# Performance work log

Measured on AMD Instinct MI355X. Metric: run time of the kernel, lower is better.

## Reference

```python
import jax, jax.numpy as jnp
import numpy as np

# dims: batch, internal ticks, neurons, input dim, NLM memory length, NLM hidden, sync pairs, out dims
B, T_TICKS, D, D_IN, M, H, P, D_OUT, D_ACT = 512, 8, 2048, 512, 16, 4, 512, 512, 512


def setup_inputs() -> dict:
    key = jax.random.key(0)
    ks = jax.random.split(key, 16)
    n = lambda k, shape: jax.random.normal(k, shape, dtype=jnp.float32)
    return {
        "x": n(ks[0], (B, D_IN)),
        # input projection
        "W_in": n(ks[1], (D_IN, D)) * 0.02,
        "b_in": jnp.zeros((D,), jnp.float32),
        # learned start post-activation state
        "z0": n(ks[2], (D,)) * 0.02,
        # synapse model: concat(z, features) -> pre-activations
        "W_syn": n(ks[3], (D + D, D)) * 0.02,
        "b_syn": jnp.zeros((D,), jnp.float32),
        # privately parameterized neuron-level models (NeuronLevelModel)
        "nlm_w1": n(ks[4], (M, H, D)) * 0.02,
        "nlm_b1": jnp.zeros((1, H, D), jnp.float32),
        "nlm_w2": n(ks[5], (H, D)) * 0.02,
        "nlm_b2": jnp.zeros((1, D), jnp.float32),
        # neural synchronization (NeuralSynchronization)
        "decay_out": jnp.zeros((P,), jnp.float32),
        "decay_action": jnp.zeros((P,), jnp.float32),
        "W_out": n(ks[6], (P, D_OUT)) * 0.02,
        "b_out": jnp.zeros((D_OUT,), jnp.float32),
        "W_act": n(ks[7], (P, D_ACT)) * 0.02,
        "b_act": jnp.zeros((D_ACT,), jnp.float32),
        # random neuron index pairs (buffers, int)
        "pairs_out": jax.random.randint(ks[8], (P, 2), 0, D),
        "pairs_action": jax.random.randint(ks[9], (P, 2), 0, D),
    }


def _nlm(hist, w1, b1, w2, b2):
    # hist: (B, D, M); private per-neuron 2-layer MLP
    h = jnp.einsum('bdM,Mhd->bdh', hist, w1) + jnp.swapaxes(b1, 1, 2)  # (B, D, H)
    h = jax.nn.relu(h)
    return jnp.einsum('bdh,hd->bd', h, w2) + b2  # (B, D)


def reference(x, W_in, b_in, z0, W_syn, b_syn, nlm_w1, nlm_b1, nlm_w2, nlm_b2,
              decay_out, decay_action, W_out, b_out, W_act, b_act,
              pairs_out, pairs_action):
    feats = x @ W_in + b_in                      # (B, D)
    z = jnp.broadcast_to(z0, (x.shape[0], D))    # (B, D)
    hist = jnp.zeros((x.shape[0], D, M), x.dtype)
    # exponential-decay sync recurrence: S_t = exp(-|r|) * S_{t-1} + z_i z_j
    # equals sum_s z_{i,s} z_{j,s} exp(-|r| (t - s))  (matches compute_sync weights)
    r_out = jnp.exp(-jnp.abs(decay_out))         # (P,)
    r_act = jnp.exp(-jnp.abs(decay_action))
    S_out = jnp.zeros((x.shape[0], P), x.dtype)
    S_act = jnp.zeros((x.shape[0], P), x.dtype)
    ys, qs = [], []
    for _ in range(T_TICKS):
        pre = jnp.concatenate([z, feats], axis=-1) @ W_syn + b_syn     # (B, D)
        hist = jnp.concatenate([hist[..., 1:], pre[..., None]], axis=-1)
        z = _nlm(hist, nlm_w1, nlm_b1, nlm_w2, nlm_b2)                 # (B, D)
        S_out = S_out * r_out + z[:, pairs_out[:, 0]] * z[:, pairs_out[:, 1]]
        S_act = S_act * r_act + z[:, pairs_action[:, 0]] * z[:, pairs_action[:, 1]]
        ys.append(S_out @ W_out + b_out)
        qs.append(S_act @ W_act + b_act)
    return jnp.stack(ys, axis=1), jnp.stack(qs, axis=1)  # (B, T, d_out), (B, T, d_action)
```

## Files before the change

kernel.cpp:

```cpp
#include <hip/hip_runtime.h>
#include <math.h>

#define Bsz 512
#define TT 8
#define Dn 2048
#define DIN 512
#define Hh 4
#define Pn 512
#define DOUT 512
#define BD (Bsz*Dn)

typedef __attribute__((ext_vector_type(8))) short s16x8;
typedef __attribute__((ext_vector_type(4))) float f32x4;
typedef __attribute__((ext_vector_type(4))) unsigned short u16x4;

__device__ __forceinline__ unsigned short f2bf(float f) {
  unsigned int u = __float_as_uint(f);
  unsigned int r = (u + 0x7fffu + ((u >> 16) & 1u)) >> 16;
  return (unsigned short)r;
}
__device__ __forceinline__ float bf2f(unsigned short h) {
  return __uint_as_float(((unsigned int)h) << 16);
}
__device__ __forceinline__ void split2(float x, unsigned short& h, unsigned short& l) {
  h = f2bf(x);
  float r = x - bf2f(h);
  l = f2bf(r);
}

#define GLOAD16(g, l) __builtin_amdgcn_global_load_lds( \
    (const __attribute__((address_space(1))) unsigned int*)(g), \
    (__attribute__((address_space(3))) unsigned int*)(l), 16, 0, 0)

__device__ __forceinline__ void gemm_core(
    const unsigned short* __restrict__ Ah, const unsigned short* __restrict__ Al,
    const unsigned short* __restrict__ BTh, const unsigned short* __restrict__ BTl,
    int K, long arow0, long brow0,
    unsigned short* LDS, f32x4 acc[2][2], int g, int qw)
{
  const int tid = threadIdx.x;
  const int lane = tid & 63;
  const int lh = lane >> 4, sc = lane & 15;
  const unsigned short* gsrc[8];
  int ldst[8];
#pragma unroll
  for (int t = 0; t < 4; ++t) {
    int rb = qw * 16 + t * 4;
    int row = rb + lh;
    int ko = ((sc & 7) ^ (row & 7)) << 3;
    gsrc[t]     = (sc >= 8 ? Al : Ah) + (size_t)(arow0 + row) * K + ko;
    ldst[t]     = rb * 128;
    gsrc[4 + t] = (sc >= 8 ? BTl : BTh) + (size_t)(brow0 + row) * K + ko;
    ldst[4 + t] = 32768 + rb * 128;
  }

  const int nI = K >> 7;

#define STAGE(ring, i_)                                              \
  {                                                                  \
    const size_t kb = ((size_t)(2 * (i_) + g)) << 6;                 \
    unsigned short* base = LDS + (g * 2 + (ring)) * 8192;            \
    GLOAD16(gsrc[0] + kb, base + ldst[0]);                           \
    GLOAD16(gsrc[1] + kb, base + ldst[1]);                           \
    GLOAD16(gsrc[2] + kb, base + ldst[2]);                           \
    GLOAD16(gsrc[3] + kb, base + ldst[3]);                           \
    GLOAD16(gsrc[4] + kb, base + ldst[4]);                           \
    GLOAD16(gsrc[5] + kb, base + ldst[5]);                           \
    GLOAD16(gsrc[6] + kb, base + ldst[6]);                           \
    GLOAD16(gsrc[7] + kb, base + ldst[7]);                           \
  }

  const int wm = (qw & 1) * 32, wn = (qw >> 1) * 32;
  const int lm = lane & 15, kg4 = lane >> 4;
  int aoh[2][2], boh[2][2];
#pragma unroll
  for (int u = 0; u < 2; ++u) {
    int kg = u * 4 + kg4;
#pragma unroll
    for (int mt = 0; mt < 2; ++mt) {
      int ar = wm + mt * 16 + lm;
      aoh[u][mt] = ar * 128 + ((kg ^ (ar & 7)) << 3);
    }
#pragma unroll
    for (int nt = 0; nt < 2; ++nt) {
      int br = wn + nt * 16 + lm;
      boh[u][nt] = br * 128 + ((kg ^ (br & 7)) << 3);
    }
  }

  STAGE(0, 0);
  for (int i = 0; i < nI; ++i) {
    asm volatile("s_waitcnt vmcnt(0)" ::: "memory");
    __builtin_amdgcn_s_barrier();
    if (i + 1 < nI) STAGE((i + 1) & 1, i + 1);
    const unsigned short* ab = LDS + (g * 2 + (i & 1)) * 8192;
    const unsigned short* bb = ab + 32768;
#pragma unroll
    for (int u = 0; u < 2; ++u) {
      s16x8 fah[2], fal[2], fbh[2], fbl[2];
#pragma unroll
      for (int mt = 0; mt < 2; ++mt) {
        fah[mt] = *(const s16x8*)(ab + aoh[u][mt]);
        fal[mt] = *(const s16x8*)(ab + aoh[u][mt] + 64);
      }
#pragma unroll
      for (int nt = 0; nt < 2; ++nt) {
        fbh[nt] = *(const s16x8*)(bb + boh[u][nt]);
        fbl[nt] = *(const s16x8*)(bb + boh[u][nt] + 64);
      }
      __builtin_amdgcn_s_setprio(1);
#pragma unroll
      for (int mt = 0; mt < 2; ++mt)
#pragma unroll
        for (int nt = 0; nt < 2; ++nt) {
          acc[mt][nt] = __builtin_amdgcn_mfma_f32_16x16x32_bf16(fah[mt], fbh[nt], acc[mt][nt], 0, 0, 0);
          acc[mt][nt] = __builtin_amdgcn_mfma_f32_16x16x32_bf16(fah[mt], fbl[nt], acc[mt][nt], 0, 0, 0);
          acc[mt][nt] = __builtin_amdgcn_mfma_f32_16x16x32_bf16(fal[mt], fbh[nt], acc[mt][nt], 0, 0, 0);
        }
      __builtin_amdgcn_s_setprio(0);
    }
  }
#undef STAGE

  __builtin_amdgcn_s_barrier();
  float* fred = (float*)LDS;
  const int ridx = (qw * 64 + lane) * 17;
  if (g == 1) {
#pragma unroll
    for (int mt = 0; mt < 2; ++mt)
#pragma unroll
      for (int nt = 0; nt < 2; ++nt)
#pragma unroll
        for (int r = 0; r < 4; ++r)
          fred[ridx + (mt * 2 + nt) * 4 + r] = acc[mt][nt][r];
  }
  __builtin_amdgcn_s_barrier();
  if (g == 0) {
#pragma unroll
    for (int mt = 0; mt < 2; ++mt)
#pragma unroll
      for (int nt = 0; nt < 2; ++nt)
#pragma unroll
        for (int r = 0; r < 4; ++r)
          acc[mt][nt][r] += fred[ridx + (mt * 2 + nt) * 4 + r];
  }
}

template<int MODE>
__global__ __launch_bounds__(512, 1)
void mfma_gemm(const unsigned short* __restrict__ Ah, const unsigned short* __restrict__ Al,
               const unsigned short* __restrict__ BTh, const unsigned short* __restrict__ BTl,
               const float* __restrict__ bias, float* __restrict__ Cf,
               unsigned short* __restrict__ Ch, unsigned short* __restrict__ Cl,
               int M, int N, int K, int gm, int gn)
{
  __shared__ unsigned short LDS[65536];
  int bid = blockIdx.x;
  int xcd = bid & 7, w = bid >> 3;
  int bmi = w % gm, bni = xcd * (gn >> 3) + w / gm;
  long bm = (long)bmi * 64, bn = (long)bni * 64;
  const int tid = threadIdx.x, lane = tid & 63, wave = tid >> 6;
  const int g = wave >> 2, qw = wave & 3;
  f32x4 acc[2][2];
#pragma unroll
  for (int a = 0; a < 2; ++a)
#pragma unroll
    for (int b = 0; b < 2; ++b) acc[a][b] = (f32x4)0.f;
  gemm_core(Ah, Al, BTh, BTl, K, bm, bn, LDS, acc, g, qw);
  if (g == 1) return;

  const int wm = (qw & 1) * 32, wn = (qw >> 1) * 32;
#pragma unroll
  for (int nt = 0; nt < 2; ++nt) {
    int n = (int)bn + wn + nt * 16 + (lane & 15);
    float bv = bias[n];
#pragma unroll
    for (int mt = 0; mt < 2; ++mt) {
      long r0 = bm + wm + mt * 16 + (lane >> 4) * 4;
#pragma unroll
      for (int r = 0; r < 4; ++r) {
        float v = acc[mt][nt][r] + bv;
        long R = r0 + r;
        if (MODE == 0) {
          unsigned short h_, l_; split2(v, h_, l_);
          Ch[R * N + n] = h_; Cl[R * N + n] = l_;
        } else if (MODE == 1) {
          Cf[R * N + n] = v;
        } else {
          long t = R >> 9, b = R & 511;
          Cf[(b * TT + t) * N + n] = v;
        }
      }
    }
  }
}

template<int TAU>
__global__ __launch_bounds__(512, 1)
void tick_mfma(const unsigned short* __restrict__ zh, const unsigned short* __restrict__ zl,
               const unsigned short* __restrict__ WTh, const unsigned short* __restrict__ WTl,
               const float* __restrict__ basep, const float* __restrict__ hist,
               float* __restrict__ histout,
               const float* __restrict__ w1, const float* __restrict__ b1,
               const float* __restrict__ w2, const float* __restrict__ b2,
               unsigned short* __restrict__ zho, unsigned short* __restrict__ zlo,
               unsigned short* __restrict__ zT)
{
  __shared__ unsigned short LDS[65536];
  int bid = blockIdx.x;
  int xcd = bid & 7, w = bid >> 3;
  int bmi = w % 8, bni = xcd * 4 + w / 8;
  long bm = (long)bmi * 64, bn = (long)bni * 64;
  const int tid = threadIdx.x, lane = tid & 63, wave = tid >> 6;
  const int g = wave >> 2, qw = wave & 3;
  f32x4 acc[2][2];
#pragma unroll
  for (int a = 0; a < 2; ++a)
#pragma unroll
    for (int b = 0; b < 2; ++b) acc[a][b] = (f32x4)0.f;
  gemm_core(zh, zl, WTh, WTl, Dn, bm, bn, LDS, acc, g, qw);
  if (g == 1) return;

  const int wm = (qw & 1) * 32, wn = (qw >> 1) * 32;
#pragma unroll
  for (int nt = 0; nt < 2; ++nt) {
    const int d = (int)bn + wn + nt * 16 + (lane & 15);
    float w2v[Hh], b1v[Hh];
#pragma unroll
    for (int hh = 0; hh < Hh; ++hh) {
      w2v[hh] = w2[hh * Dn + d];
      b1v[hh] = b1[hh * Dn + d];
    }
    const float b2v = b2[d];
#pragma unroll
    for (int mt = 0; mt < 2; ++mt) {
      const int b0 = (int)bm + wm + mt * 16 + (lane >> 4) * 4;
      float pre[4], hacc[4][Hh];
#pragma unroll
      for (int r = 0; r < 4; ++r) {
        pre[r] = acc[mt][nt][r] + basep[(size_t)(b0 + r) * Dn + d];
#pragma unroll
        for (int hh = 0; hh < Hh; ++hh) hacc[r][hh] = b1v[hh];
      }
#pragma unroll
      for (int s = 0; s < TAU; ++s) {
        float wv[Hh];
#pragma unroll
        for (int hh = 0; hh < Hh; ++hh) wv[hh] = w1[((15 - TAU + s) * Hh + hh) * Dn + d];
#pragma unroll
        for (int r = 0; r < 4; ++r) {
          float psv = hist[(size_t)s * BD + (size_t)(b0 + r) * Dn + d];
#pragma unroll
          for (int hh = 0; hh < Hh; ++hh) hacc[r][hh] = fmaf(psv, wv[hh], hacc[r][hh]);
        }
      }
      {
        float wv[Hh];
#pragma unroll
        for (int hh = 0; hh < Hh; ++hh) wv[hh] = w1[(15 * Hh + hh) * Dn + d];
#pragma unroll
        for (int r = 0; r < 4; ++r)
#pragma unroll
          for (int hh = 0; hh < Hh; ++hh) hacc[r][hh] = fmaf(pre[r], wv[hh], hacc[r][hh]);
      }
      u16x4 pack;
#pragma unroll
      for (int r = 0; r < 4; ++r) {
        histout[(size_t)(b0 + r) * Dn + d] = pre[r];
        float z = b2v;
#pragma unroll
        for (int hh = 0; hh < Hh; ++hh) z = fmaf(fmaxf(hacc[r][hh], 0.f), w2v[hh], z);
        unsigned short h_, l_; split2(z, h_, l_);
        zho[(size_t)(b0 + r) * Dn + d] = h_;
        zlo[(size_t)(b0 + r) * Dn + d] = l_;
        pack[r] = f2bf(z);
      }
      *(u16x4*)&zT[(size_t)d * Bsz + b0] = pack;
    }
  }
}

__global__ __launch_bounds__(256)
void tick0_kernel(const float* __restrict__ basep, const float* __restrict__ q,
                  float* __restrict__ histout,
                  const float* __restrict__ w1, const float* __restrict__ b1,
                  const float* __restrict__ w2, const float* __restrict__ b2,
                  unsigned short* __restrict__ zho, unsigned short* __restrict__ zlo,
                  unsigned short* __restrict__ zT)
{
  int g = blockIdx.x * 256 + threadIdx.x;
  int b = g >> 8;
  int d0 = (g & 255) * 8;
#pragma unroll
  for (int k = 0; k < 8; ++k) {
    int d = d0 + k;
    float pre = basep[(size_t)b * Dn + d] + q[d];
    histout[(size_t)b * Dn + d] = pre;
    float z = b2[d];
#pragma unroll
    for (int hh = 0; hh < Hh; ++hh) {
      float h = fmaf(pre, w1[(15 * Hh + hh) * Dn + d], b1[hh * Dn + d]);
      z = fmaf(fmaxf(h, 0.f), w2[hh * Dn + d], z);
    }
    unsigned short h_, l_; split2(z, h_, l_);
    zho[(size_t)b * Dn + d] = h_;
    zlo[(size_t)b * Dn + d] = l_;
    zT[(size_t)d * Bsz + b] = f2bf(z);
  }
}

__global__ __launch_bounds__(512)
void sync_kernel(const unsigned short* __restrict__ zT,
                 const int* __restrict__ pairs0, const int* __restrict__ pairs1,
                 const float* __restrict__ decay0, const float* __restrict__ decay1,
                 unsigned short* __restrict__ Sh0, unsigned short* __restrict__ Sl0,
                 unsigned short* __restrict__ Sh1, unsigned short* __restrict__ Sl1)
{
  __shared__ float Ls[8][8][65];
  const int set = blockIdx.y;
  const int* pairs = set ? pairs1 : pairs0;
  const float* decay = set ? decay1 : decay0;
  unsigned short* Sh = set ? Sh1 : Sh0;
  unsigned short* Sl = set ? Sl1 : Sl0;
  const int tid = threadIdx.x;
  const int lb = tid & 63, pl = tid >> 6;
  const int p = blockIdx.x * 8 + pl;
  const int i = pairs[2 * p], j = pairs[2 * p + 1];
  const float r = expf(-fabsf(decay[p]));
  const int pb = tid & 7, bb2 = tid >> 3;
  for (int bb = 0; bb < 8; ++bb) {
    int b = bb * 64 + lb;
    float S = 0.f, St[8];
#pragma unroll
    for (int t = 0; t < 8; ++t) {
      float zi = bf2f(zT[(size_t)t * BD + (size_t)i * Bsz + b]);
      float zj = bf2f(zT[(size_t)t * BD + (size_t)j * Bsz + b]);
      S = fmaf(S, r, zi * zj);
      St[t] = S;
    }
#pragma unroll
    for (int t = 0; t < 8; ++t) Ls[pl][t][lb] = St[t];
    __syncthreads();
#pragma unroll
    for (int t = 0; t < 8; ++t) {
      float v = Ls[pb][t][bb2];
      unsigned short h_, l_; split2(v, h_, l_);
      size_t off = ((size_t)t * Bsz + bb * 64 + bb2) * Pn + blockIdx.x * 8 + pb;
      Sh[off] = h_; Sl[off] = l_;
    }
    __syncthreads();
  }
}

__global__ __launch_bounds__(256)
void transpose_split_kernel(const float* __restrict__ in, int ldin,
                            unsigned short* __restrict__ Th, unsigned short* __restrict__ Tl,
                            int K)
{
  __shared__ float T[64][65];
  int k0 = blockIdx.x * 64, n0 = blockIdx.y * 64;
  int tid = threadIdx.x;
  int r = tid >> 2, c0 = (tid & 3) * 16;
#pragma unroll
  for (int cc = 0; cc < 16; cc += 4) {
    float4 v = *(const float4*)(in + (size_t)(k0 + r) * ldin + n0 + c0 + cc);
    T[c0 + cc + 0][r] = v.x; T[c0 + cc + 1][r] = v.y;
    T[c0 + cc + 2][r] = v.z; T[c0 + cc + 3][r] = v.w;
  }
  __syncthreads();
  int n = tid >> 2, kc = (tid & 3) * 16;
#pragma unroll
  for (int kk = 0; kk < 16; ++kk) {
    float v = T[n][kc + kk];
    unsigned short h_, l_; split2(v, h_, l_);
    Th[(size_t)(n0 + n) * K + k0 + kc + kk] = h_;
    Tl[(size_t)(n0 + n) * K + k0 + kc + kk] = l_;
  }
}

__global__ __launch_bounds__(256)
void split_kernel(const float* __restrict__ x, unsigned short* __restrict__ xh,
                  unsigned short* __restrict__ xl, int n4)
{
  int i = blockIdx.x * 256 + threadIdx.x;
  if (i >= n4) return;
  float4 v = *(const float4*)(x + (size_t)i * 4);
  u16x4 h, l;
  unsigned short th, tl;
  split2(v.x, th, tl); h[0] = th; l[0] = tl;
  split2(v.y, th, tl); h[1] = th; l[1] = tl;
  split2(v.z, th, tl); h[2] = th; l[2] = tl;
  split2(v.w, th, tl); h[3] = th; l[3] = tl;
  *(u16x4*)(xh + (size_t)i * 4) = h;
  *(u16x4*)(xl + (size_t)i * 4) = l;
}

__global__ __launch_bounds__(256)
void matvec_part_kernel(const float* __restrict__ vec, const float* __restrict__ W,
                        float* __restrict__ part, int K, int N)
{
  __shared__ float red[4][64];
  const int tid = threadIdx.x;
  const int c = tid & 63, strip = tid >> 6;
  const int col = blockIdx.x * 64 + c;
  const int kpc = K / (gridDim.y * 4);
  const int k0 = (blockIdx.y * 4 + strip) * kpc;
  float acc = 0.f;
#pragma unroll 8
  for (int k = k0; k < k0 + kpc; ++k)
    acc = fmaf(vec[k], W[(size_t)k * N + col], acc);
  red[strip][c] = acc;
  __syncthreads();
  if (strip == 0)
    part[(size_t)blockIdx.y * N + col] = red[0][c] + red[1][c] + red[2][c] + red[3][c];
}

__global__ __launch_bounds__(256)
void reduce_q_kernel(const float* __restrict__ part, float* __restrict__ q, int N, int C)
{
  int d = blockIdx.x * 256 + threadIdx.x;
  if (d >= N) return;
  float s = 0.f;
  for (int c = 0; c < C; ++c) s += part[(size_t)c * N + d];
  q[d] = s;
}

extern "C" void kernel_launch(void* const* d_in, const int* in_sizes, int n_in,
                              void* d_out, int out_size, void* d_ws, size_t ws_size,
                              hipStream_t stream) {
  const float* x      = (const float*)d_in[0];
  const float* W_in   = (const float*)d_in[1];
  const float* b_in   = (const float*)d_in[2];
  const float* z0     = (const float*)d_in[3];
  const float* W_syn  = (const float*)d_in[4];
  const float* b_syn  = (const float*)d_in[5];
  const float* w1     = (const float*)d_in[6];
  const float* b1     = (const float*)d_in[7];
  const float* w2     = (const float*)d_in[8];
  const float* b2     = (const float*)d_in[9];
  const float* decay_out = (const float*)d_in[10];
  const float* decay_act = (const float*)d_in[11];
  const float* W_out  = (const float*)d_in[12];
  const float* b_out  = (const float*)d_in[13];
  const float* W_act  = (const float*)d_in[14];
  const float* b_act  = (const float*)d_in[15];
  const int* pairs_out = (const int*)d_in[16];
  const int* pairs_act = (const int*)d_in[17];

  char* W = (char*)d_ws;
  auto alloc = [&](size_t bytes) { char* p = W; W += (bytes + 255) & ~255ull; return p; };
  unsigned short* WtTh = (unsigned short*)alloc((size_t)Dn * Dn * 2);
  unsigned short* WtTl = (unsigned short*)alloc((size_t)Dn * Dn * 2);
  unsigned short* WbTh = (unsigned short*)alloc((size_t)Dn * Dn * 2);
  unsigned short* WbTl = (unsigned short*)alloc((size_t)Dn * Dn * 2);
  unsigned short* WinTh = (unsigned short*)alloc((size_t)Dn * DIN * 2);
  unsigned short* WinTl = (unsigned short*)alloc((size_t)Dn * DIN * 2);
  unsigned short* WoTh = (unsigned short*)alloc((size_t)DOUT * Pn * 2);
  unsigned short* WoTl = (unsigned short*)alloc((size_t)DOUT * Pn * 2);
  unsigned short* WaTh = (unsigned short*)alloc((size_t)DOUT * Pn * 2);
  unsigned short* WaTl = (unsigned short*)alloc((size_t)DOUT * Pn * 2);
  unsigned short* xh = (unsigned short*)alloc((size_t)Bsz * DIN * 2);
  unsigned short* xl = (unsigned short*)alloc((size_t)Bsz * DIN * 2);
  unsigned short* fh = (unsigned short*)alloc((size_t)BD * 2);
  unsigned short* fl = (unsigned short*)alloc((size_t)BD * 2);
  float* q     = (float*)alloc(Dn * 4);
  float* qpart = (float*)alloc(8 * Dn * 4);
  float* base  = (float*)alloc((size_t)BD * 4);
  float* hist  = (float*)alloc((size_t)TT * BD * 4);
  unsigned short* zbh[2], *zbl[2];
  zbh[0] = (unsigned short*)alloc((size_t)BD * 2);
  zbl[0] = (unsigned short*)alloc((size_t)BD * 2);
  zbh[1] = (unsigned short*)alloc((size_t)BD * 2);
  zbl[1] = (unsigned short*)alloc((size_t)BD * 2);
  unsigned short* zT = (unsigned short*)alloc((size_t)TT * BD * 2);
  unsigned short* Sh0 = WbTh;
  unsigned short* Sl0 = WbTh + (size_t)TT * Bsz * Pn;
  unsigned short* Sh1 = WbTl;
  unsigned short* Sl1 = WbTl + (size_t)TT * Bsz * Pn;

  float* outy = (float*)d_out;
  float* outq = outy + (size_t)Bsz * TT * DOUT;

  dim3 blk(256);
  dim3 blk512(512);
  transpose_split_kernel<<<dim3(32, 32), blk, 0, stream>>>(W_syn, Dn, WtTh, WtTl, Dn);
  transpose_split_kernel<<<dim3(32, 32), blk, 0, stream>>>(W_syn + (size_t)Dn * Dn, Dn, WbTh, WbTl, Dn);
  transpose_split_kernel<<<dim3(8, 32), blk, 0, stream>>>(W_in, Dn, WinTh, WinTl, DIN);
  transpose_split_kernel<<<dim3(8, 8), blk, 0, stream>>>(W_out, DOUT, WoTh, WoTl, Pn);
  transpose_split_kernel<<<dim3(8, 8), blk, 0, stream>>>(W_act, DOUT, WaTh, WaTl, Pn);
  split_kernel<<<dim3(Bsz * DIN / 1024), blk, 0, stream>>>(x, xh, xl, Bsz * DIN / 4);
  matvec_part_kernel<<<dim3(Dn / 64, 8), blk, 0, stream>>>(z0, W_syn, qpart, Dn, Dn);
  reduce_q_kernel<<<dim3(Dn / 256), blk, 0, stream>>>(qpart, q, Dn, 8);
  mfma_gemm<0><<<dim3(256), blk512, 0, stream>>>(xh, xl, WinTh, WinTl, b_in, nullptr, fh, fl,
                                                 Bsz, Dn, DIN, 8, 32);
  mfma_gemm<1><<<dim3(256), blk512, 0, stream>>>(fh, fl, WbTh, WbTl, b_syn, base, nullptr, nullptr,
                                                 Bsz, Dn, Dn, 8, 32);
  tick0_kernel<<<dim3(512), blk, 0, stream>>>(base, q, hist, w1, b1, w2, b2,
                                              zbh[0], zbl[0], zT);
  for (int tau = 1; tau < TT; ++tau) {
    const unsigned short* zih = zbh[(tau + 1) & 1];
    const unsigned short* zil = zbl[(tau + 1) & 1];
    unsigned short* zoh = zbh[tau & 1];
    unsigned short* zol = zbl[tau & 1];
    float* ho = hist + (size_t)tau * BD;
    unsigned short* zTo = zT + (size_t)tau * BD;
    switch (tau) {
      case 1: tick_mfma<1><<<dim3(256), blk512, 0, stream>>>(zih, zil, WtTh, WtTl, base, hist, ho, w1, b1, w2, b2, zoh, zol, zTo); break;
      case 2: tick_mfma<2><<<dim3(256), blk512, 0, stream>>>(zih, zil, WtTh, WtTl, base, hist, ho, w1, b1, w2, b2, zoh, zol, zTo); break;
      case 3: tick_mfma<3><<<dim3(256), blk512, 0, stream>>>(zih, zil, WtTh, WtTl, base, hist, ho, w1, b1, w2, b2, zoh, zol, zTo); break;
      case 4: tick_mfma<4><<<dim3(256), blk512, 0, stream>>>(zih, zil, WtTh, WtTl, base, hist, ho, w1, b1, w2, b2, zoh, zol, zTo); break;
      case 5: tick_mfma<5><<<dim3(256), blk512, 0, stream>>>(zih, zil, WtTh, WtTl, base, hist, ho, w1, b1, w2, b2, zoh, zol, zTo); break;
      case 6: tick_mfma<6><<<dim3(256), blk512, 0, stream>>>(zih, zil, WtTh, WtTl, base, hist, ho, w1, b1, w2, b2, zoh, zol, zTo); break;
      case 7: tick_mfma<7><<<dim3(256), blk512, 0, stream>>>(zih, zil, WtTh, WtTl, base, hist, ho, w1, b1, w2, b2, zoh, zol, zTo); break;
    }
  }
  sync_kernel<<<dim3(Pn / 8, 2), dim3(512), 0, stream>>>(zT, pairs_out, pairs_act,
                                                         decay_out, decay_act,
                                                         Sh0, Sl0, Sh1, Sl1);
  mfma_gemm<2><<<dim3(512), blk512, 0, stream>>>(Sh0, Sl0, WoTh, WoTl, b_out, outy, nullptr, nullptr,
                                                 TT * Bsz, DOUT, Pn, 64, 8);
  mfma_gemm<2><<<dim3(512), blk512, 0, stream>>>(Sh1, Sl1, WaTh, WaTl, b_act, outq, nullptr, nullptr,
                                                 TT * Bsz, DOUT, Pn, 64, 8);
}
```

Before: 314.5 us.

## Fuse tick pipeline into persistent kernel with grid barriers and merge prep kernels

Replaces the feature GEMM, base GEMM, tick0 and seven per-tick kernel launches with one persistent 256-block kernel that advances through the stages using a software grid barrier built on atomics. The separate transpose, split and matvec prep kernels are merged into a single launch, and the q reduction is folded into tick 0. The aim is to cut launch overhead and inter-kernel gaps across the serial tick chain. In exchange the code relies on all 256 blocks being co-resident, adds spin-wait barrier cost, and turns the per-tick history loop from a compile-time template into a runtime loop.

```diff
diff --git a/kernel.cpp b/kernel.cpp
--- a/kernel.cpp
+++ b/kernel.cpp
@@ -59,15 +59,15 @@
 #define STAGE(ring, i_)                                              \
   {                                                                  \
     const size_t kb = ((size_t)(2 * (i_) + g)) << 6;                 \
-    unsigned short* base = LDS + (g * 2 + (ring)) * 8192;            \
-    GLOAD16(gsrc[0] + kb, base + ldst[0]);                           \
-    GLOAD16(gsrc[1] + kb, base + ldst[1]);                           \
-    GLOAD16(gsrc[2] + kb, base + ldst[2]);                           \
-    GLOAD16(gsrc[3] + kb, base + ldst[3]);                           \
-    GLOAD16(gsrc[4] + kb, base + ldst[4]);                           \
-    GLOAD16(gsrc[5] + kb, base + ldst[5]);                           \
-    GLOAD16(gsrc[6] + kb, base + ldst[6]);                           \
-    GLOAD16(gsrc[7] + kb, base + ldst[7]);                           \
+    unsigned short* base_ = LDS + (g * 2 + (ring)) * 8192;           \
+    GLOAD16(gsrc[0] + kb, base_ + ldst[0]);                          \
+    GLOAD16(gsrc[1] + kb, base_ + ldst[1]);                          \
+    GLOAD16(gsrc[2] + kb, base_ + ldst[2]);                          \
+    GLOAD16(gsrc[3] + kb, base_ + ldst[3]);                          \
+    GLOAD16(gsrc[4] + kb, base_ + ldst[4]);                          \
+    GLOAD16(gsrc[5] + kb, base_ + ldst[5]);                          \
+    GLOAD16(gsrc[6] + kb, base_ + ldst[6]);                          \
+    GLOAD16(gsrc[7] + kb, base_ + ldst[7]);                          \
   }
 
   const int wm = (qw & 1) * 32, wn = (qw >> 1) * 32;
@@ -143,6 +143,213 @@
 #pragma unroll
         for (int r = 0; r < 4; ++r)
           acc[mt][nt][r] += fred[ridx + (mt * 2 + nt) * 4 + r];
+  }
+}
+
+__device__ __forceinline__ void grid_barrier(unsigned* bar) {
+  __syncthreads();
+  if (threadIdx.x == 0) {
+    __threadfence();
+    unsigned g = __hip_atomic_load(bar + 1, __ATOMIC_RELAXED, __HIP_MEMORY_SCOPE_AGENT);
+    unsigned a = __hip_atomic_fetch_add(bar, 1u, __ATOMIC_ACQ_REL, __HIP_MEMORY_SCOPE_AGENT);
+    if (a == 255u) {
+      __hip_atomic_store(bar, 0u, __ATOMIC_RELAXED, __HIP_MEMORY_SCOPE_AGENT);
+      __hip_atomic_store(bar + 1, g + 1u, __ATOMIC_RELEASE, __HIP_MEMORY_SCOPE_AGENT);
+    } else {
+      while (__hip_atomic_load(bar + 1, __ATOMIC_ACQUIRE, __HIP_MEMORY_SCOPE_AGENT) == g)
+        __builtin_amdgcn_s_sleep(2);
+    }
+    __threadfence();
+  }
+  __syncthreads();
+}
+
+__global__ __launch_bounds__(512, 1)
+void mega_kernel(const unsigned short* __restrict__ xh, const unsigned short* __restrict__ xl,
+                 const unsigned short* __restrict__ WinTh, const unsigned short* __restrict__ WinTl,
+                 const float* __restrict__ b_in,
+                 unsigned short* __restrict__ fh, unsigned short* __restrict__ fl,
+                 const unsigned short* __restrict__ WbTh, const unsigned short* __restrict__ WbTl,
+                 const float* __restrict__ b_syn, float* __restrict__ basep,
+                 const float* __restrict__ qpart,
+                 const unsigned short* __restrict__ WtTh, const unsigned short* __restrict__ WtTl,
+                 const float* __restrict__ w1, const float* __restrict__ b1,
+                 const float* __restrict__ w2, const float* __restrict__ b2,
+                 float* __restrict__ hist,
+                 unsigned short* __restrict__ zh0, unsigned short* __restrict__ zl0,
+                 unsigned short* __restrict__ zh1, unsigned short* __restrict__ zl1,
+                 unsigned short* __restrict__ zT,
+                 unsigned* bar)
+{
+  __shared__ unsigned short LDS[65536];
+  const int bid = blockIdx.x;
+  const int xcd = bid & 7, w = bid >> 3;
+  const int bmi = w % 8, bni = xcd * 4 + w / 8;
+  const long bm = (long)bmi * 64, bn = (long)bni * 64;
+  const int tid = threadIdx.x, lane = tid & 63, wave = tid >> 6;
+  const int g = wave >> 2, qw = wave & 3;
+  const int wm = (qw & 1) * 32, wn = (qw >> 1) * 32;
+
+  {
+    f32x4 acc[2][2];
+#pragma unroll
+    for (int a = 0; a < 2; ++a)
+#pragma unroll
+      for (int b = 0; b < 2; ++b) acc[a][b] = (f32x4)0.f;
+    gemm_core(xh, xl, WinTh, WinTl, DIN, bm, bn, LDS, acc, g, qw);
+    if (g == 0) {
+#pragma unroll
+      for (int nt = 0; nt < 2; ++nt) {
+        int n = (int)bn + wn + nt * 16 + (lane & 15);
+        float bv = b_in[n];
+#pragma unroll
+        for (int mt = 0; mt < 2; ++mt) {
+          long r0 = bm + wm + mt * 16 + (lane >> 4) * 4;
+#pragma unroll
+          for (int r = 0; r < 4; ++r) {
+            float v = acc[mt][nt][r] + bv;
+            unsigned short h_, l_; split2(v, h_, l_);
+            fh[(r0 + r) * Dn + n] = h_; fl[(r0 + r) * Dn + n] = l_;
+          }
+        }
+      }
+    }
+  }
+  grid_barrier(bar);
+
+  {
+    f32x4 acc[2][2];
+#pragma unroll
+    for (int a = 0; a < 2; ++a)
+#pragma unroll
+      for (int b = 0; b < 2; ++b) acc[a][b] = (f32x4)0.f;
+    gemm_core(fh, fl, WbTh, WbTl, Dn, bm, bn, LDS, acc, g, qw);
+    if (g == 0) {
+#pragma unroll
+      for (int nt = 0; nt < 2; ++nt) {
+        int n = (int)bn + wn + nt * 16 + (lane & 15);
+        float bv = b_syn[n];
+#pragma unroll
+        for (int mt = 0; mt < 2; ++mt) {
+          long r0 = bm + wm + mt * 16 + (lane >> 4) * 4;
+#pragma unroll
+          for (int r = 0; r < 4; ++r)
+            basep[(r0 + r) * Dn + n] = acc[mt][nt][r] + bv;
+        }
+      }
+    }
+  }
+  grid_barrier(bar);
+
+  {
+    float* Q = (float*)LDS;
+    Q[(tid >> 6) * 64 + (tid & 63)] = qpart[(size_t)(tid >> 6) * Dn + bn + (tid & 63)];
+    __syncthreads();
+    const int dl = tid & 63;
+    const int d = (int)bn + dl;
+    float qv = 0.f;
+#pragma unroll
+    for (int c = 0; c < 8; ++c) qv += Q[c * 64 + dl];
+    float w1v[Hh], b1v[Hh], w2v[Hh];
+#pragma unroll
+    for (int hh = 0; hh < Hh; ++hh) {
+      w1v[hh] = w1[(15 * Hh + hh) * Dn + d];
+      b1v[hh] = b1[hh * Dn + d];
+      w2v[hh] = w2[hh * Dn + d];
+    }
+    const float b2v = b2[d];
+#pragma unroll
+    for (int k = 0; k < 8; ++k) {
+      int b = (int)bm + (tid >> 6) + k * 8;
+      float pre = basep[(size_t)b * Dn + d] + qv;
+      hist[(size_t)b * Dn + d] = pre;
+      float z = b2v;
+#pragma unroll
+      for (int hh = 0; hh < Hh; ++hh) {
+        float h = fmaf(pre, w1v[hh], b1v[hh]);
+        z = fmaf(fmaxf(h, 0.f), w2v[hh], z);
+      }
+      unsigned short h_, l_; split2(z, h_, l_);
+      zh0[(size_t)b * Dn + d] = h_;
+      zl0[(size_t)b * Dn + d] = l_;
+      zT[(size_t)d * Bsz + b] = f2bf(z);
+    }
+  }
+  grid_barrier(bar);
+
+  for (int tau = 1; tau < TT; ++tau) {
+    const unsigned short *zih, *zil;
+    unsigned short *zoh, *zol;
+    if (tau & 1) { zih = zh0; zil = zl0; zoh = zh1; zol = zl1; }
+    else         { zih = zh1; zil = zl1; zoh = zh0; zol = zl0; }
+    float* ho = hist + (size_t)tau * BD;
+    unsigned short* zTo = zT + (size_t)tau * BD;
+
+    f32x4 acc[2][2];
+#pragma unroll
+    for (int a = 0; a < 2; ++a)
+#pragma unroll
+      for (int b = 0; b < 2; ++b) acc[a][b] = (f32x4)0.f;
+    gemm_core(zih, zil, WtTh, WtTl, Dn, bm, bn, LDS, acc, g, qw);
+
+    if (g == 0) {
+#pragma unroll
+      for (int nt = 0; nt < 2; ++nt) {
+        const int d = (int)bn + wn + nt * 16 + (lane & 15);
+        float w2v[Hh], b1v[Hh];
+#pragma unroll
+        for (int hh = 0; hh < Hh; ++hh) {
+          w2v[hh] = w2[hh * Dn + d];
+          b1v[hh] = b1[hh * Dn + d];
+        }
+        const float b2v = b2[d];
+#pragma unroll
+        for (int mt = 0; mt < 2; ++mt) {
+          const int b0 = (int)bm + wm + mt * 16 + (lane >> 4) * 4;
+          float pre[4], hacc[4][Hh];
+#pragma unroll
+          for (int r = 0; r < 4; ++r) {
+            pre[r] = acc[mt][nt][r] + basep[(size_t)(b0 + r) * Dn + d];
+#pragma unroll
+            for (int hh = 0; hh < Hh; ++hh) hacc[r][hh] = b1v[hh];
+          }
+          for (int s = 0; s < tau; ++s) {
+            float wv[Hh];
+#pragma unroll
+            for (int hh = 0; hh < Hh; ++hh) wv[hh] = w1[((15 - tau + s) * Hh + hh) * Dn + d];
+#pragma unroll
+            for (int r = 0; r < 4; ++r) {
+              float psv = hist[(size_t)s * BD + (size_t)(b0 + r) * Dn + d];
+#pragma unroll
+              for (int hh = 0; hh < Hh; ++hh) hacc[r][hh] = fmaf(psv, wv[hh], hacc[r][hh]);
+            }
+          }
+          {
+            float wv[Hh];
+#pragma unroll
+            for (int hh = 0; hh < Hh; ++hh) wv[hh] = w1[(15 * Hh + hh) * Dn + d];
+#pragma unroll
+            for (int r = 0; r < 4; ++r)
+#pragma unroll
+              for (int hh = 0; hh < Hh; ++hh) hacc[r][hh] = fmaf(pre[r], wv[hh], hacc[r][hh]);
+          }
+          u16x4 pack;
+#pragma unroll
+          for (int r = 0; r < 4; ++r) {
+            ho[(size_t)(b0 + r) * Dn + d] = pre[r];
+            float z = b2v;
+#pragma unroll
+            for (int hh = 0; hh < Hh; ++hh) z = fmaf(fmaxf(hacc[r][hh], 0.f), w2v[hh], z);
+            unsigned short h_, l_; split2(z, h_, l_);
+            zoh[(size_t)(b0 + r) * Dn + d] = h_;
+            zol[(size_t)(b0 + r) * Dn + d] = l_;
+            pack[r] = f2bf(z);
+          }
+          *(u16x4*)&zTo[(size_t)d * Bsz + b0] = pack;
+        }
+      }
+    }
+    if (tau < TT - 1) grid_barrier(bar);
   }
 }
 
@@ -192,120 +399,6 @@
         }
       }
     }
-  }
-}
-
-template<int TAU>
-__global__ __launch_bounds__(512, 1)
-void tick_mfma(const unsigned short* __restrict__ zh, const unsigned short* __restrict__ zl,
-               const unsigned short* __restrict__ WTh, const unsigned short* __restrict__ WTl,
-               const float* __restrict__ basep, const float* __restrict__ hist,
-               float* __restrict__ histout,
-               const float* __restrict__ w1, const float* __restrict__ b1,
-               const float* __restrict__ w2, const float* __restrict__ b2,
-               unsigned short* __restrict__ zho, unsigned short* __restrict__ zlo,
-               unsigned short* __restrict__ zT)
-{
-  __shared__ unsigned short LDS[65536];
-  int bid = blockIdx.x;
-  int xcd = bid & 7, w = bid >> 3;
-  int bmi = w % 8, bni = xcd * 4 + w / 8;
-  long bm = (long)bmi * 64, bn = (long)bni * 64;
-  const int tid = threadIdx.x, lane = tid & 63, wave = tid >> 6;
-  const int g = wave >> 2, qw = wave & 3;
-  f32x4 acc[2][2];
-#pragma unroll
-  for (int a = 0; a < 2; ++a)
-#pragma unroll
-    for (int b = 0; b < 2; ++b) acc[a][b] = (f32x4)0.f;
-  gemm_core(zh, zl, WTh, WTl, Dn, bm, bn, LDS, acc, g, qw);
-  if (g == 1) return;
-
-  const int wm = (qw & 1) * 32, wn = (qw >> 1) * 32;
-#pragma unroll
-  for (int nt = 0; nt < 2; ++nt) {
-    const int d = (int)bn + wn + nt * 16 + (lane & 15);
-    float w2v[Hh], b1v[Hh];
-#pragma unroll
-    for (int hh = 0; hh < Hh; ++hh) {
-      w2v[hh] = w2[hh * Dn + d];
-      b1v[hh] = b1[hh * Dn + d];
-    }
-    const float b2v = b2[d];
-#pragma unroll
-    for (int mt = 0; mt < 2; ++mt) {
-      const int b0 = (int)bm + wm + mt * 16 + (lane >> 4) * 4;
-      float pre[4], hacc[4][Hh];
-#pragma unroll
-      for (int r = 0; r < 4; ++r) {
-        pre[r] = acc[mt][nt][r] + basep[(size_t)(b0 + r) * Dn + d];
-#pragma unroll
-        for (int hh = 0; hh < Hh; ++hh) hacc[r][hh] = b1v[hh];
-      }
-#pragma unroll
-      for (int s = 0; s < TAU; ++s) {
-        float wv[Hh];
-#pragma unroll
-        for (int hh = 0; hh < Hh; ++hh) wv[hh] = w1[((15 - TAU + s) * Hh + hh) * Dn + d];
-#pragma unroll
-        for (int r = 0; r < 4; ++r) {
-          float psv = hist[(size_t)s * BD + (size_t)(b0 + r) * Dn + d];
-#pragma unroll
-          for (int hh = 0; hh < Hh; ++hh) hacc[r][hh] = fmaf(psv, wv[hh], hacc[r][hh]);
-        }
-      }
-      {
-        float wv[Hh];
-#pragma unroll
-        for (int hh = 0; hh < Hh; ++hh) wv[hh] = w1[(15 * Hh + hh) * Dn + d];
-#pragma unroll
-        for (int r = 0; r < 4; ++r)
-#pragma unroll
-          for (int hh = 0; hh < Hh; ++hh) hacc[r][hh] = fmaf(pre[r], wv[hh], hacc[r][hh]);
-      }
-      u16x4 pack;
-#pragma unroll
-      for (int r = 0; r < 4; ++r) {
-        histout[(size_t)(b0 + r) * Dn + d] = pre[r];
-        float z = b2v;
-#pragma unroll
-        for (int hh = 0; hh < Hh; ++hh) z = fmaf(fmaxf(hacc[r][hh], 0.f), w2v[hh], z);
-        unsigned short h_, l_; split2(z, h_, l_);
-        zho[(size_t)(b0 + r) * Dn + d] = h_;
-        zlo[(size_t)(b0 + r) * Dn + d] = l_;
-        pack[r] = f2bf(z);
-      }
-      *(u16x4*)&zT[(size_t)d * Bsz + b0] = pack;
-    }
-  }
-}
-
-__global__ __launch_bounds__(256)
-void tick0_kernel(const float* __restrict__ basep, const float* __restrict__ q,
-                  float* __restrict__ histout,
-                  const float* __restrict__ w1, const float* __restrict__ b1,
-                  const float* __restrict__ w2, const float* __restrict__ b2,
-                  unsigned short* __restrict__ zho, unsigned short* __restrict__ zlo,
-                  unsigned short* __restrict__ zT)
-{
-  int g = blockIdx.x * 256 + threadIdx.x;
-  int b = g >> 8;
-  int d0 = (g & 255) * 8;
-#pragma unroll
-  for (int k = 0; k < 8; ++k) {
-    int d = d0 + k;
-    float pre = basep[(size_t)b * Dn + d] + q[d];
-    histout[(size_t)b * Dn + d] = pre;
-    float z = b2[d];
-#pragma unroll
-    for (int hh = 0; hh < Hh; ++hh) {
-      float h = fmaf(pre, w1[(15 * Hh + hh) * Dn + d], b1[hh * Dn + d]);
-      z = fmaf(fmaxf(h, 0.f), w2[hh * Dn + d], z);
-    }
-    unsigned short h_, l_; split2(z, h_, l_);
-    zho[(size_t)b * Dn + d] = h_;
-    zlo[(size_t)b * Dn + d] = l_;
-    zT[(size_t)d * Bsz + b] = f2bf(z);
   }
 }
 
@@ -352,13 +445,11 @@
   }
 }
 
-__global__ __launch_bounds__(256)
-void transpose_split_kernel(const float* __restrict__ in, int ldin,
-                            unsigned short* __restrict__ Th, unsigned short* __restrict__ Tl,
-                            int K)
+__device__ __forceinline__ void transpose_tile(const float* __restrict__ in, int ldin,
+    unsigned short* __restrict__ Th, unsigned short* __restrict__ Tl, int K,
+    int kb, int nb, float T[64][65])
 {
-  __shared__ float T[64][65];
-  int k0 = blockIdx.x * 64, n0 = blockIdx.y * 64;
+  int k0 = kb * 64, n0 = nb * 64;
   int tid = threadIdx.x;
   int r = tid >> 2, c0 = (tid & 3) * 16;
 #pragma unroll
@@ -379,50 +470,61 @@
 }
 
 __global__ __launch_bounds__(256)
-void split_kernel(const float* __restrict__ x, unsigned short* __restrict__ xh,
-                  unsigned short* __restrict__ xl, int n4)
+void prep_kernel(const float* __restrict__ W_syn, const float* __restrict__ W_in,
+                 const float* __restrict__ W_out, const float* __restrict__ W_act,
+                 const float* __restrict__ x, const float* __restrict__ z0,
+                 unsigned short* WtTh, unsigned short* WtTl,
+                 unsigned short* WbTh, unsigned short* WbTl,
+                 unsigned short* WinTh, unsigned short* WinTl,
+                 unsigned short* WoTh, unsigned short* WoTl,
+                 unsigned short* WaTh, unsigned short* WaTl,
+                 unsigned short* xh, unsigned short* xl,
+                 float* qpart)
 {
-  int i = blockIdx.x * 256 + threadIdx.x;
-  if (i >= n4) return;
-  float4 v = *(const float4*)(x + (size_t)i * 4);
-  u16x4 h, l;
-  unsigned short th, tl;
-  split2(v.x, th, tl); h[0] = th; l[0] = tl;
-  split2(v.y, th, tl); h[1] = th; l[1] = tl;
-  split2(v.z, th, tl); h[2] = th; l[2] = tl;
-  split2(v.w, th, tl); h[3] = th; l[3] = tl;
-  *(u16x4*)(xh + (size_t)i * 4) = h;
-  *(u16x4*)(xl + (size_t)i * 4) = l;
-}
-
-__global__ __launch_bounds__(256)
-void matvec_part_kernel(const float* __restrict__ vec, const float* __restrict__ W,
-                        float* __restrict__ part, int K, int N)
-{
-  __shared__ float red[4][64];
+  __shared__ float T[64][65];
+  const int b = blockIdx.x;
   const int tid = threadIdx.x;
-  const int c = tid & 63, strip = tid >> 6;
-  const int col = blockIdx.x * 64 + c;
-  const int kpc = K / (gridDim.y * 4);
-  const int k0 = (blockIdx.y * 4 + strip) * kpc;
-  float acc = 0.f;
+  if (b < 1024) {
+    transpose_tile(W_syn, Dn, WtTh, WtTl, Dn, b & 31, b >> 5, T);
+  } else if (b < 2048) {
+    int b2 = b - 1024;
+    transpose_tile(W_syn + (size_t)Dn * Dn, Dn, WbTh, WbTl, Dn, b2 & 31, b2 >> 5, T);
+  } else if (b < 2304) {
+    int b2 = b - 2048;
+    transpose_tile(W_in, Dn, WinTh, WinTl, DIN, b2 & 7, b2 >> 3, T);
+  } else if (b < 2368) {
+    int b2 = b - 2304;
+    transpose_tile(W_out, DOUT, WoTh, WoTl, Pn, b2 & 7, b2 >> 3, T);
+  } else if (b < 2432) {
+    int b2 = b - 2368;
+    transpose_tile(W_act, DOUT, WaTh, WaTl, Pn, b2 & 7, b2 >> 3, T);
+  } else if (b < 2688) {
+    int i = (b - 2432) * 256 + tid;
+    float4 v = *(const float4*)(x + (size_t)i * 4);
+    u16x4 h, l;
+    unsigned short th, tl;
+    split2(v.x, th, tl); h[0] = th; l[0] = tl;
+    split2(v.y, th, tl); h[1] = th; l[1] = tl;
+    split2(v.z, th, tl); h[2] = th; l[2] = tl;
+    split2(v.w, th, tl); h[3] = th; l[3] = tl;
+    *(u16x4*)(xh + (size_t)i * 4) = h;
+    *(u16x4*)(xl + (size_t)i * 4) = l;
+  } else {
+    int idx = b - 2688;
+    int colb = idx & 31, kc = idx >> 5;
+    float (*red)[64] = (float(*)[64])T;
+    const int c = tid & 63, strip = tid >> 6;
+    const int col = colb * 64 + c;
+    const int k0 = (kc * 4 + strip) * 64;
+    float acc = 0.f;
 #pragma unroll 8
-  for (int k = k0; k < k0 + kpc; ++k)
-    acc = fmaf(vec[k], W[(size_t)k * N + col], acc);
-  red[strip][c] = acc;
-  __syncthreads();
-  if (strip == 0)
-    part[(size_t)blockIdx.y * N + col] = red[0][c] + red[1][c] + red[2][c] + red[3][c];
-}
-
-__global__ __launch_bounds__(256)
-void reduce_q_kernel(const float* __restrict__ part, float* __restrict__ q, int N, int C)
-{
-  int d = blockIdx.x * 256 + threadIdx.x;
-  if (d >= N) return;
-  float s = 0.f;
-  for (int c = 0; c < C; ++c) s += part[(size_t)c * N + d];
-  q[d] = s;
+    for (int k = k0; k < k0 + 64; ++k)
+      acc = fmaf(z0[k], W_syn[(size_t)k * Dn + col], acc);
+    red[strip][c] = acc;
+    __syncthreads();
+    if (strip == 0)
+      qpart[(size_t)kc * Dn + col] = red[0][c] + red[1][c] + red[2][c] + red[3][c];
+  }
 }
 
 extern "C" void kernel_launch(void* const* d_in, const int* in_sizes, int n_in,
@@ -473,52 +575,31 @@
   zbh[1] = (unsigned short*)alloc((size_t)BD * 2);
   zbl[1] = (unsigned short*)alloc((size_t)BD * 2);
   unsigned short* zT = (unsigned short*)alloc((size_t)TT * BD * 2);
+  unsigned* bar = (unsigned*)alloc(256);
   unsigned short* Sh0 = WbTh;
   unsigned short* Sl0 = WbTh + (size_t)TT * Bsz * Pn;
   unsigned short* Sh1 = WbTl;
   unsigned short* Sl1 = WbTl + (size_t)TT * Bsz * Pn;
+  (void)q;
 
   float* outy = (float*)d_out;
   float* outq = outy + (size_t)Bsz * TT * DOUT;
 
-  dim3 blk(256);
-  dim3 blk512(512);
-  transpose_split_kernel<<<dim3(32, 32), blk, 0, stream>>>(W_syn, Dn, WtTh, WtTl, Dn);
-  transpose_split_kernel<<<dim3(32, 32), blk, 0, stream>>>(W_syn + (size_t)Dn * Dn, Dn, WbTh, WbTl, Dn);
-  transpose_split_kernel<<<dim3(8, 32), blk, 0, stream>>>(W_in, Dn, WinTh, WinTl, DIN);
-  transpose_split_kernel<<<dim3(8, 8), blk, 0, stream>>>(W_out, DOUT, WoTh, WoTl, Pn);
-  transpose_split_kernel<<<dim3(8, 8), blk, 0, stream>>>(W_act, DOUT, WaTh, WaTl, Pn);
-  split_kernel<<<dim3(Bsz * DIN / 1024), blk, 0, stream>>>(x, xh, xl, Bsz * DIN / 4);
-  matvec_part_kernel<<<dim3(Dn / 64, 8), blk, 0, stream>>>(z0, W_syn, qpart, Dn, Dn);
-  reduce_q_kernel<<<dim3(Dn / 256), blk, 0, stream>>>(qpart, q, Dn, 8);
-  mfma_gemm<0><<<dim3(256), blk512, 0, stream>>>(xh, xl, WinTh, WinTl, b_in, nullptr, fh, fl,
-                                                 Bsz, Dn, DIN, 8, 32);
-  mfma_gemm<1><<<dim3(256), blk512, 0, stream>>>(fh, fl, WbTh, WbTl, b_syn, base, nullptr, nullptr,
-                                                 Bsz, Dn, Dn, 8, 32);
-  tick0_kernel<<<dim3(512), blk, 0, stream>>>(base, q, hist, w1, b1, w2, b2,
-                                              zbh[0], zbl[0], zT);
-  for (int tau = 1; tau < TT; ++tau) {
-    const unsigned short* zih = zbh[(tau + 1) & 1];
-    const unsigned short* zil = zbl[(tau + 1) & 1];
-    unsigned short* zoh = zbh[tau & 1];
-    unsigned short* zol = zbl[tau & 1];
-    float* ho = hist + (size_t)tau * BD;
-    unsigned short* zTo = zT + (size_t)tau * BD;
-    switch (tau) {
-      case 1: tick_mfma<1><<<dim3(256), blk512, 0, stream>>>(zih, zil, WtTh, WtTl, base, hist, ho, w1, b1, w2, b2, zoh, zol, zTo); break;
-      case 2: tick_mfma<2><<<dim3(256), blk512, 0, stream>>>(zih, zil, WtTh, WtTl, base, hist, ho, w1, b1, w2, b2, zoh, zol, zTo); break;
-      case 3: tick_mfma<3><<<dim3(256), blk512, 0, stream>>>(zih, zil, WtTh, WtTl, base, hist, ho, w1, b1, w2, b2, zoh, zol, zTo); break;
-      case 4: tick_mfma<4><<<dim3(256), blk512, 0, stream>>>(zih, zil, WtTh, WtTl, base, hist, ho, w1, b1, w2, b2, zoh, zol, zTo); break;
-      case 5: tick_mfma<5><<<dim3(256), blk512, 0, stream>>>(zih, zil, WtTh, WtTl, base, hist, ho, w1, b1, w2, b2, zoh, zol, zTo); break;
-      case 6: tick_mfma<6><<<dim3(256), blk512, 0, stream>>>(zih, zil, WtTh, WtTl, base, hist, ho, w1, b1, w2, b2, zoh, zol, zTo); break;
-      case 7: tick_mfma<7><<<dim3(256), blk512, 0, stream>>>(zih, zil, WtTh, WtTl, base, hist, ho, w1, b1, w2, b2, zoh, zol, zTo); break;
-    }
-  }
+  hipMemsetAsync(bar, 0, 8, stream);
+  prep_kernel<<<dim3(2944), dim3(256), 0, stream>>>(
+      W_syn, W_in, W_out, W_act, x, z0,
+      WtTh, WtTl, WbTh, WbTl, WinTh, WinTl, WoTh, WoTl, WaTh, WaTl,
+      xh, xl, qpart);
+  mega_kernel<<<dim3(256), dim3(512), 0, stream>>>(
+      xh, xl, WinTh, WinTl, b_in, fh, fl,
+      WbTh, WbTl, b_syn, base, qpart, WtTh, WtTl,
+      w1, b1, w2, b2, hist,
+      zbh[0], zbl[0], zbh[1], zbl[1], zT, bar);
   sync_kernel<<<dim3(Pn / 8, 2), dim3(512), 0, stream>>>(zT, pairs_out, pairs_act,
                                                          decay_out, decay_act,
                                                          Sh0, Sl0, Sh1, Sl1);
-  mfma_gemm<2><<<dim3(512), blk512, 0, stream>>>(Sh0, Sl0, WoTh, WoTl, b_out, outy, nullptr, nullptr,
-                                                 TT * Bsz, DOUT, Pn, 64, 8);
-  mfma_gemm<2><<<dim3(512), blk512, 0, stream>>>(Sh1, Sl1, WaTh, WaTl, b_act, outq, nullptr, nullptr,
-                                                 TT * Bsz, DOUT, Pn, 64, 8);
-}
+  mfma_gemm<2><<<dim3(512), dim3(512), 0, stream>>>(Sh0, Sl0, WoTh, WoTl, b_out, outy, nullptr, nullptr,
+                                                    TT * Bsz, DOUT, Pn, 64, 8);
+  mfma_gemm<2><<<dim3(512), dim3(512), 0, stream>>>(Sh1, Sl1, WaTh, WaTl, b_act, outq, nullptr, nullptr,
+                                                    TT * Bsz, DOUT, Pn, 64, 8);
+}
```

New measurement: 759.7 us. 2.42x slower.
